# Kernel optimization log

Measured on AMD Instinct MI355X. Metric: run time of the kernel, lower is better.

## Reference

```python
import jax, jax.numpy as jnp
import numpy as np

D = 1024
H = 16


def setup_inputs() -> dict:
    key = jax.random.key(0)
    ks = jax.random.split(key, 5)
    s = 1.0 / np.sqrt(D)
    x = jax.random.normal(ks[0], (4, 1024, D), dtype=jnp.float32)
    W_qkv = jax.random.normal(ks[1], (D, 3 * D), dtype=jnp.float32) * s
    b_qkv = jnp.zeros((3 * D,), dtype=jnp.float32)
    W_out = jax.random.normal(ks[2], (D, D), dtype=jnp.float32) * s
    b_out = jnp.zeros((D,), dtype=jnp.float32)
    return {"x": x, "W_qkv": W_qkv, "b_qkv": b_qkv, "W_out": W_out, "b_out": b_out}


def reference(x, W_qkv, b_qkv, W_out, b_out):
    bs, ns, d = x.shape
    dh = d // H
    scale = 1.0 / np.sqrt(dh)
    qkv = x @ W_qkv + b_qkv                      # [B,S,3D]
    qkv = qkv.reshape(bs, ns, 3, H, dh)
    q, k, v = qkv[:, :, 0], qkv[:, :, 1], qkv[:, :, 2]  # [B,S,H,dh]
    # attention scores [B,H,S,S]
    attn = jnp.einsum('bqhd,bkhd->bhqk', q, k) * scale
    attn = jax.nn.softmax(attn, axis=-1)
    out = jnp.einsum('bhqk,bkhd->bqhd', attn, v)  # [B,S,H,dh]
    out = out.reshape(bs, ns, d)
    return out @ W_out + b_out
```

## Files before the change

kernel.cpp:

```cpp
#include <hip/hip_runtime.h>
#include <hip/hip_bf16.h>
#include <cstdint>

typedef __bf16 bf16x8 __attribute__((ext_vector_type(8)));
typedef float f32x4 __attribute__((ext_vector_type(4)));

__device__ __forceinline__ unsigned short f2b(float f) {
  __bf16 h = (__bf16)f;
  return __builtin_bit_cast(unsigned short, h);
}

__device__ __forceinline__ void gload_lds16(const void* g, void* l) {
  __builtin_amdgcn_global_load_lds(
      (__attribute__((address_space(1))) void*)g,
      (__attribute__((address_space(3))) void*)l,
      16, 0, 0);
}

__global__ void cvt_f32_bf16(const float* __restrict__ in,
                             unsigned short* __restrict__ out, int n) {
  int i = (blockIdx.x * blockDim.x + threadIdx.x) * 4;
  if (i + 3 < n) {
    float4 f = *(const float4*)&in[i];
    ushort4 u = make_ushort4(f2b(f.x), f2b(f.y), f2b(f.z), f2b(f.w));
    *(ushort4*)&out[i] = u;
  }
}

__global__ void transpose_cvt(const float* __restrict__ in,
                              unsigned short* __restrict__ out, int R, int C) {
  __shared__ float tile[32][33];
  int c0 = blockIdx.x * 32, r0 = blockIdx.y * 32;
  int x = threadIdx.x, y = threadIdx.y;
  #pragma unroll
  for (int j = y; j < 32; j += 8)
    tile[j][x] = in[(size_t)(r0 + j) * C + c0 + x];
  __syncthreads();
  #pragma unroll
  for (int j = y; j < 32; j += 8)
    out[(size_t)(c0 + j) * R + r0 + x] = f2b(tile[x][j]);
}

__global__ void transpose_v(const unsigned short* __restrict__ qkv,
                            unsigned short* __restrict__ vt) {
  __shared__ unsigned short tile[32][33];
  int bh = blockIdx.x, s0 = blockIdx.y * 32, d0 = blockIdx.z * 32;
  int b = bh >> 4, h = bh & 15;
  int x = threadIdx.x, y = threadIdx.y;
  #pragma unroll
  for (int j = y; j < 32; j += 8)
    tile[j][x] = qkv[(size_t)(b * 1024 + s0 + j) * 3072 + 2048 + h * 64 + d0 + x];
  __syncthreads();
  #pragma unroll
  for (int j = y; j < 32; j += 8)
    vt[(size_t)(bh * 64 + d0 + j) * 1024 + s0 + x] = tile[x][j];
}

template <int OUT_F32>
__global__ __launch_bounds__(256, 2)
void gemm_bt(const unsigned short* __restrict__ A,
             const unsigned short* __restrict__ Bt,
             const float* __restrict__ bias, void* __restrict__ C,
             int M, int N, int K) {
  __shared__ __align__(16) unsigned short sA[2][128 * 32];
  __shared__ __align__(16) unsigned short sB[2][128 * 32];
  const int t = threadIdx.x;
  const int w = t >> 6, lane = t & 63;
  const int ln = lane & 15, lq = lane >> 4;
  const int wr = w >> 1, wc = w & 1;
  const int m0 = blockIdx.y * 128, n0 = blockIdx.x * 128;

  f32x4 acc[4][4];
  #pragma unroll
  for (int i = 0; i < 4; i++)
    #pragma unroll
    for (int j = 0; j < 4; j++) acc[i][j] = (f32x4){0.f, 0.f, 0.f, 0.f};

  auto stage = [&](int buf, int k0) {
    #pragma unroll
    for (int i = 0; i < 2; ++i) {
      int idx = i * 256 + t;
      int row = idx >> 2;
      int cb = (idx & 3) * 8;
      gload_lds16(A + (size_t)(m0 + row) * K + k0 + cb, &sA[buf][idx * 8]);
    }
    #pragma unroll
    for (int i = 0; i < 2; ++i) {
      int idx = i * 256 + t;
      int row = idx >> 2;
      int cb = (idx & 3) * 8;
      gload_lds16(Bt + (size_t)(n0 + row) * K + k0 + cb, &sB[buf][idx * 8]);
    }
  };

  stage(0, 0);
  asm volatile("s_waitcnt vmcnt(0)" ::: "memory");
  __builtin_amdgcn_s_barrier();

  const int nk = K >> 5;
  for (int ki = 0; ki < nk; ++ki) {
    const int cur = ki & 1;
    if (ki + 1 < nk) stage(cur ^ 1, (ki + 1) << 5);

    bf16x8 af[4], bfr[4];
    #pragma unroll
    for (int m = 0; m < 4; m++)
      af[m] = *(const bf16x8*)&sA[cur][(wr * 64 + m * 16 + ln) * 32 + lq * 8];
    #pragma unroll
    for (int n = 0; n < 4; n++)
      bfr[n] = *(const bf16x8*)&sB[cur][(wc * 64 + n * 16 + ln) * 32 + lq * 8];
    __builtin_amdgcn_s_setprio(1);
    #pragma unroll
    for (int m = 0; m < 4; m++)
      #pragma unroll
      for (int n = 0; n < 4; n++)
        acc[m][n] = __builtin_amdgcn_mfma_f32_16x16x32_bf16(af[m], bfr[n], acc[m][n], 0, 0, 0);
    __builtin_amdgcn_s_setprio(0);

    asm volatile("s_waitcnt vmcnt(0)" ::: "memory");
    __builtin_amdgcn_s_barrier();
  }

  #pragma unroll
  for (int m = 0; m < 4; m++) {
    #pragma unroll
    for (int n = 0; n < 4; n++) {
      int col = n0 + wc * 64 + n * 16 + ln;
      float bv = bias[col];
      #pragma unroll
      for (int r = 0; r < 4; r++) {
        int row = m0 + wr * 64 + m * 16 + lq * 4 + r;
        float v = acc[m][n][r] + bv;
        if (OUT_F32)
          ((float*)C)[(size_t)row * N + col] = v;
        else
          ((unsigned short*)C)[(size_t)row * N + col] = f2b(v);
      }
    }
  }
}

__global__ __launch_bounds__(256, 4)
void attn_fwd(const unsigned short* __restrict__ qkv,
              const unsigned short* __restrict__ vt,
              unsigned short* __restrict__ aout) {
  const int b = blockIdx.z, h = blockIdx.y, q0 = blockIdx.x * 64;
  __shared__ __align__(16) unsigned short sB[4][64 * 64];
  __shared__ __align__(16) unsigned short sP[4][16 * 64];
  const int t = threadIdx.x;
  const int w = t >> 6, lane = t & 63;
  const int ln = lane & 15, lq = lane >> 4;
  const float K2 = 0.125f * 1.44269504f;
  const float THR = 11.54f;

  const size_t qbase = (size_t)(b * 1024 + q0) * 3072 + h * 64;
  const size_t kbase = (size_t)(b * 1024) * 3072 + 1024 + h * 64;
  const size_t vbase = (size_t)((b * 16 + h) * 64) * 1024;

  #pragma unroll
  for (int i = 0; i < 2; i++) {
    int idx = i * 256 + t;
    int row = idx >> 3, ch = idx & 7;
    int sw = (ch ^ (row & 7)) * 8;
    gload_lds16(qkv + qbase + (size_t)row * 3072 + sw, &sB[0][idx * 8]);
    gload_lds16(qkv + kbase + (size_t)row * 3072 + sw, &sB[1][idx * 8]);
    gload_lds16(vt + vbase + (size_t)row * 1024 + sw, &sB[2][idx * 8]);
  }
  __syncthreads();
  bf16x8 qf[2];
  #pragma unroll
  for (int c = 0; c < 2; c++) {
    int row = w * 16 + ln;
    qf[c] = *(const bf16x8*)&sB[0][row * 64 + ((c * 4 + lq) ^ (ln & 7)) * 8];
  }
  __syncthreads();

  f32x4 o[4];
  float mrow = -1e30f, lsum = 0.f;
  #pragma unroll
  for (int n = 0; n < 4; n++) o[n] = (f32x4){0.f, 0.f, 0.f, 0.f};

  for (int kt = 0; kt < 16; ++kt) {
    const unsigned short* kb = sB[(kt & 1) ? 3 : 1];
    const unsigned short* vb = sB[(kt & 1) ? 0 : 2];
    if (kt < 15) {
      const int kv1 = (kt + 1) * 64;
      unsigned short* kn = sB[(kt & 1) ? 1 : 3];
      unsigned short* vn = sB[(kt & 1) ? 2 : 0];
      #pragma unroll
      for (int i = 0; i < 2; i++) {
        int idx = i * 256 + t;
        int row = idx >> 3, ch = idx & 7;
        int sw = (ch ^ (row & 7)) * 8;
        gload_lds16(qkv + kbase + (size_t)(kv1 + row) * 3072 + sw, &kn[idx * 8]);
        gload_lds16(vt + vbase + (size_t)row * 1024 + kv1 + sw, &vn[idx * 8]);
      }
    }

    f32x4 st[4];
    #pragma unroll
    for (int kc = 0; kc < 4; kc++) {
      int krow = kc * 16 + ln;
      bf16x8 k0f = *(const bf16x8*)&kb[krow * 64 + ((0 + lq) ^ (ln & 7)) * 8];
      bf16x8 k1f = *(const bf16x8*)&kb[krow * 64 + ((4 + lq) ^ (ln & 7)) * 8];
      __builtin_amdgcn_s_setprio(1);
      st[kc] = __builtin_amdgcn_mfma_f32_16x16x32_bf16(k0f, qf[0], (f32x4){0.f, 0.f, 0.f, 0.f}, 0, 0, 0);
      st[kc] = __builtin_amdgcn_mfma_f32_16x16x32_bf16(k1f, qf[1], st[kc], 0, 0, 0);
      __builtin_amdgcn_s_setprio(0);
    }

    float xv[4][4];
    float tm = -1e30f;
    #pragma unroll
    for (int kc = 0; kc < 4; kc++) {
      #pragma unroll
      for (int r = 0; r < 4; r++) {
        xv[kc][r] = st[kc][r] * K2;
        tm = fmaxf(tm, xv[kc][r]);
      }
    }
    tm = fmaxf(tm, __shfl_xor(tm, 16));
    tm = fmaxf(tm, __shfl_xor(tm, 32));

    if (!__all(tm <= mrow + THR)) {
      float mn = fmaxf(mrow, tm);
      float al = exp2f(mrow - mn);
      mrow = mn;
      lsum *= al;
      #pragma unroll
      for (int r = 0; r < 4; r++) {
        float alr = __shfl(al, (lane & 48) | (lq * 4 + r));
        #pragma unroll
        for (int n = 0; n < 4; n++) o[n][r] *= alr;
      }
    }

    float ts = 0.f;
    #pragma unroll
    for (int kc = 0; kc < 4; kc++) {
      #pragma unroll
      for (int r = 0; r < 4; r++) {
        xv[kc][r] = exp2f(xv[kc][r] - mrow);
        ts += xv[kc][r];
      }
    }
    ts += __shfl_xor(ts, 16);
    ts += __shfl_xor(ts, 32);
    lsum += ts;

    unsigned char* pb = (unsigned char*)sP[w];
    #pragma unroll
    for (int kc = 0; kc < 4; kc++) {
      ushort4 u = make_ushort4(f2b(xv[kc][0]), f2b(xv[kc][1]),
                               f2b(xv[kc][2]), f2b(xv[kc][3]));
      int boff = (kc * 32 + lq * 8) ^ ((ln & 7) << 4);
      *(ushort4*)(pb + ln * 128 + boff) = u;
    }

    #pragma unroll
    for (int c2 = 0; c2 < 2; c2++) {
      bf16x8 pa = *(const bf16x8*)&sP[w][ln * 64 + ((c2 * 4 + lq) ^ (ln & 7)) * 8];
      __builtin_amdgcn_s_setprio(1);
      #pragma unroll
      for (int n = 0; n < 4; n++) {
        int vrow = n * 16 + ln;
        bf16x8 vf = *(const bf16x8*)&vb[vrow * 64 + ((c2 * 4 + lq) ^ (ln & 7)) * 8];
        o[n] = __builtin_amdgcn_mfma_f32_16x16x32_bf16(pa, vf, o[n], 0, 0, 0);
      }
      __builtin_amdgcn_s_setprio(0);
    }

    asm volatile("s_waitcnt vmcnt(0)" ::: "memory");
    __builtin_amdgcn_s_barrier();
  }

  float linv[4];
  #pragma unroll
  for (int r = 0; r < 4; r++)
    linv[r] = 1.f / __shfl(lsum, (lane & 48) | (lq * 4 + r));
  #pragma unroll
  for (int n = 0; n < 4; n++) {
    #pragma unroll
    for (int r = 0; r < 4; r++) {
      int row = q0 + w * 16 + lq * 4 + r;
      int col = h * 64 + n * 16 + ln;
      aout[(size_t)(b * 1024 + row) * 1024 + col] = f2b(o[n][r] * linv[r]);
    }
  }
}

extern "C" void kernel_launch(void* const* d_in, const int* in_sizes, int n_in,
                              void* d_out, int out_size, void* d_ws, size_t ws_size,
                              hipStream_t stream) {
  const float* x = (const float*)d_in[0];
  const float* W_qkv = (const float*)d_in[1];
  const float* b_qkv = (const float*)d_in[2];
  const float* W_out = (const float*)d_in[3];
  const float* b_out = (const float*)d_in[4];
  float* out = (float*)d_out;

  char* ws = (char*)d_ws;
  unsigned short* xb    = (unsigned short*)(ws);
  unsigned short* wqkvT = (unsigned short*)(ws + 8388608);
  unsigned short* woutT = (unsigned short*)(ws + 14680064);
  unsigned short* qkv   = (unsigned short*)(ws + 16777216);
  unsigned short* vt    = (unsigned short*)(ws + 41943040);
  unsigned short* aout  = (unsigned short*)(ws + 50331648);
  if (ws_size < 58720256) return;

  cvt_f32_bf16<<<4096, 256, 0, stream>>>(x, xb, 4096 * 1024);
  transpose_cvt<<<dim3(96, 32), dim3(32, 8), 0, stream>>>(W_qkv, wqkvT, 1024, 3072);
  transpose_cvt<<<dim3(32, 32), dim3(32, 8), 0, stream>>>(W_out, woutT, 1024, 1024);
  gemm_bt<0><<<dim3(24, 32), 256, 0, stream>>>(xb, wqkvT, b_qkv, qkv, 4096, 3072, 1024);
  transpose_v<<<dim3(64, 32, 2), dim3(32, 8), 0, stream>>>(qkv, vt);
  attn_fwd<<<dim3(16, 16, 4), 256, 0, stream>>>(qkv, vt, aout);
  gemm_bt<1><<<dim3(8, 32), 256, 0, stream>>>(aout, woutT, b_out, out, 4096, 1024, 1024);
}
```

Baseline: 126.1 us.

## Replace QKV projection GEMM with 256x256-tile, 8-wave, phase-pipelined kernel

Adds a new bf16 GEMM for the QKV projection that uses 256x256 output tiles, 512 threads and 64-wide K steps. LDS is double-buffered and XOR-swizzled, and the A/B loads are split into four phases interleaved with MFMA blocks under setprio and explicit waitcnt/barriers. Workgroup IDs are remapped so blocks spread across the 8 XCDs. The aim is more data reuse per LDS load and overlap of global-to-LDS traffic with matrix math. The cost is a grid of only 192 blocks on a 256-CU device, large LDS use (128KB), and heavy register pressure.

Result: no change. 126.4 us (+0.2%).

```diff
diff --git a/kernel.cpp b/kernel.cpp
--- a/kernel.cpp
+++ b/kernel.cpp
@@ -54,6 +54,166 @@
   #pragma unroll
   for (int j = y; j < 32; j += 8)
     vt[(size_t)(bh * 64 + d0 + j) * 1024 + s0 + x] = tile[x][j];
+}
+
+__global__ __launch_bounds__(512, 2)
+void gemm256_8ph(const unsigned short* __restrict__ Ag,
+                 const unsigned short* __restrict__ Bt,
+                 const float* __restrict__ bias,
+                 unsigned short* __restrict__ C,
+                 int M, int N, int K) {
+  __shared__ __align__(16) unsigned short sA[2][256 * 64];
+  __shared__ __align__(16) unsigned short sB[2][256 * 64];
+  const int t = threadIdx.x;
+  const int wid = t >> 6, lane = t & 63;
+  const int ln = lane & 15, lq = lane >> 4;
+  const int wm = wid >> 2, wn = wid & 3;
+
+  const int nwg = gridDim.x;
+  const int cpx = nwg >> 3;
+  const int wg = (blockIdx.x & 7) * cpx + (blockIdx.x >> 3);
+  const int nbx = N >> 8;
+  const int m0 = (wg / nbx) * 256, n0 = (wg % nbx) * 256;
+
+  f32x4 acc[8][4];
+  #pragma unroll
+  for (int i = 0; i < 8; i++)
+    #pragma unroll
+    for (int j = 0; j < 4; j++) acc[i][j] = (f32x4){0.f, 0.f, 0.f, 0.f};
+
+  auto stageA = [&](int buf, int kt, int h) {
+    #pragma unroll
+    for (int g = 0; g < 2; g++) {
+      int idx = g * 512 + t;
+      int row = h * 128 + (idx >> 3), ch = idx & 7;
+      gload_lds16(Ag + (size_t)(m0 + row) * K + kt * 64 + ((ch ^ (row & 7)) * 8),
+                  &sA[buf][h * 8192 + idx * 8]);
+    }
+  };
+  auto stageB = [&](int buf, int kt, int h) {
+    #pragma unroll
+    for (int g = 0; g < 2; g++) {
+      int idx = g * 512 + t;
+      int row = h * 128 + (idx >> 3), ch = idx & 7;
+      gload_lds16(Bt + (size_t)(n0 + row) * K + kt * 64 + ((ch ^ (row & 7)) * 8),
+                  &sB[buf][h * 8192 + idx * 8]);
+    }
+  };
+
+  const int nt = K >> 6;
+
+  stageA(0, 0, 0); stageA(0, 0, 1);
+  stageB(0, 0, 0); stageB(0, 0, 1);
+  if (nt > 1) { stageB(1, 1, 0); stageB(1, 1, 1); }
+  if (nt > 1) asm volatile("s_waitcnt vmcnt(4)" ::: "memory");
+  else        asm volatile("s_waitcnt vmcnt(0)" ::: "memory");
+  __builtin_amdgcn_s_barrier();
+
+  bf16x8 af[8], bf01[4], bf23[4];
+
+  for (int T = 0; T < nt; ++T) {
+    const int cur = T & 1, nxt = cur ^ 1;
+
+    #pragma unroll
+    for (int i = 0; i < 4; i++)
+      #pragma unroll
+      for (int kk = 0; kk < 2; kk++)
+        af[i * 2 + kk] = *(const bf16x8*)&sA[cur][(wm * 128 + i * 16 + ln) * 64 +
+                                                  ((kk * 4 + lq) ^ (ln & 7)) * 8];
+    #pragma unroll
+    for (int j = 0; j < 2; j++)
+      #pragma unroll
+      for (int kk = 0; kk < 2; kk++)
+        bf01[j * 2 + kk] = *(const bf16x8*)&sB[cur][(wn * 64 + j * 16 + ln) * 64 +
+                                                    ((kk * 4 + lq) ^ (ln & 7)) * 8];
+    if (T + 1 < nt) stageA(nxt, T + 1, 0);
+    __builtin_amdgcn_s_barrier();
+    asm volatile("s_waitcnt lgkmcnt(0)" ::: "memory");
+    __builtin_amdgcn_sched_barrier(0);
+    __builtin_amdgcn_s_setprio(1);
+    #pragma unroll
+    for (int i = 0; i < 4; i++)
+      #pragma unroll
+      for (int j = 0; j < 2; j++)
+        #pragma unroll
+        for (int kk = 0; kk < 2; kk++)
+          acc[i][j] = __builtin_amdgcn_mfma_f32_16x16x32_bf16(af[i * 2 + kk], bf01[j * 2 + kk], acc[i][j], 0, 0, 0);
+    __builtin_amdgcn_s_setprio(0);
+    __builtin_amdgcn_s_barrier();
+
+    #pragma unroll
+    for (int j = 0; j < 2; j++)
+      #pragma unroll
+      for (int kk = 0; kk < 2; kk++)
+        bf23[j * 2 + kk] = *(const bf16x8*)&sB[cur][(wn * 64 + (2 + j) * 16 + ln) * 64 +
+                                                    ((kk * 4 + lq) ^ (ln & 7)) * 8];
+    if (T + 1 < nt) stageA(nxt, T + 1, 1);
+    __builtin_amdgcn_s_barrier();
+    asm volatile("s_waitcnt lgkmcnt(0)" ::: "memory");
+    __builtin_amdgcn_sched_barrier(0);
+    __builtin_amdgcn_s_setprio(1);
+    #pragma unroll
+    for (int i = 0; i < 4; i++)
+      #pragma unroll
+      for (int j = 0; j < 2; j++)
+        #pragma unroll
+        for (int kk = 0; kk < 2; kk++)
+          acc[i][2 + j] = __builtin_amdgcn_mfma_f32_16x16x32_bf16(af[i * 2 + kk], bf23[j * 2 + kk], acc[i][2 + j], 0, 0, 0);
+    __builtin_amdgcn_s_setprio(0);
+    __builtin_amdgcn_s_barrier();
+
+    #pragma unroll
+    for (int i = 0; i < 4; i++)
+      #pragma unroll
+      for (int kk = 0; kk < 2; kk++)
+        af[i * 2 + kk] = *(const bf16x8*)&sA[cur][(wm * 128 + (4 + i) * 16 + ln) * 64 +
+                                                  ((kk * 4 + lq) ^ (ln & 7)) * 8];
+    if (T + 2 < nt) stageB(cur, T + 2, 0);
+    __builtin_amdgcn_s_barrier();
+    asm volatile("s_waitcnt lgkmcnt(0)" ::: "memory");
+    __builtin_amdgcn_sched_barrier(0);
+    __builtin_amdgcn_s_setprio(1);
+    #pragma unroll
+    for (int i = 0; i < 4; i++)
+      #pragma unroll
+      for (int j = 0; j < 2; j++)
+        #pragma unroll
+        for (int kk = 0; kk < 2; kk++)
+          acc[4 + i][j] = __builtin_amdgcn_mfma_f32_16x16x32_bf16(af[i * 2 + kk], bf01[j * 2 + kk], acc[4 + i][j], 0, 0, 0);
+    __builtin_amdgcn_s_setprio(0);
+    __builtin_amdgcn_s_barrier();
+
+    if (T + 2 < nt) stageB(cur, T + 2, 1);
+    if (T + 2 < nt)      asm volatile("s_waitcnt vmcnt(4)" ::: "memory");
+    else if (T + 1 < nt) asm volatile("s_waitcnt vmcnt(0)" ::: "memory");
+    __builtin_amdgcn_s_barrier();
+    asm volatile("s_waitcnt lgkmcnt(0)" ::: "memory");
+    __builtin_amdgcn_sched_barrier(0);
+    __builtin_amdgcn_s_setprio(1);
+    #pragma unroll
+    for (int i = 0; i < 4; i++)
+      #pragma unroll
+      for (int j = 0; j < 2; j++)
+        #pragma unroll
+        for (int kk = 0; kk < 2; kk++)
+          acc[4 + i][2 + j] = __builtin_amdgcn_mfma_f32_16x16x32_bf16(af[i * 2 + kk], bf23[j * 2 + kk], acc[4 + i][2 + j], 0, 0, 0);
+    __builtin_amdgcn_s_setprio(0);
+    __builtin_amdgcn_s_barrier();
+  }
+
+  #pragma unroll
+  for (int m = 0; m < 8; m++) {
+    #pragma unroll
+    for (int n = 0; n < 4; n++) {
+      int col = n0 + wn * 64 + n * 16 + ln;
+      float bv = bias[col];
+      #pragma unroll
+      for (int r = 0; r < 4; r++) {
+        int row = m0 + wm * 128 + m * 16 + lq * 4 + r;
+        C[(size_t)row * N + col] = f2b(acc[m][n][r] + bv);
+      }
+    }
+  }
 }
 
 template <int OUT_F32>
@@ -311,7 +471,7 @@
   cvt_f32_bf16<<<4096, 256, 0, stream>>>(x, xb, 4096 * 1024);
   transpose_cvt<<<dim3(96, 32), dim3(32, 8), 0, stream>>>(W_qkv, wqkvT, 1024, 3072);
   transpose_cvt<<<dim3(32, 32), dim3(32, 8), 0, stream>>>(W_out, woutT, 1024, 1024);
-  gemm_bt<0><<<dim3(24, 32), 256, 0, stream>>>(xb, wqkvT, b_qkv, qkv, 4096, 3072, 1024);
+  gemm256_8ph<<<192, 512, 0, stream>>>(xb, wqkvT, b_qkv, qkv, 4096, 3072, 1024);
   transpose_v<<<dim3(64, 32, 2), dim3(32, 8), 0, stream>>>(qkv, vt);
   attn_fwd<<<dim3(16, 16, 4), 256, 0, stream>>>(qkv, vt, aout);
   gemm_bt<1><<<dim3(8, 32), 256, 0, stream>>>(aout, woutT, b_out, out, 4096, 1024, 1024);
```
